# Kernel optimization log

Hardware: AMD Instinct MI355X
Metric: run time of the kernel (lower is better)

The kernel has to match this reference:

```python
import jax, jax.numpy as jnp
import numpy as np

K_SELECTED = 8  # config.num_selected_heads


def setup_inputs() -> dict:
    key = jax.random.key(0)
    k1, k2 = jax.random.split(key, 2)
    B, N, H, L = 4, 4096, 2048, 64
    x = jax.random.normal(k1, (B, N, H), dtype=jnp.float32)
    W_r = jax.random.normal(k2, (L, H), dtype=jnp.float32) * 0.02  # nn.Linear weight (L, H), no bias
    expert_bias = jnp.zeros((L,), dtype=jnp.float32)
    active_mask = jnp.ones((B, N), dtype=bool)
    return {"x": x, "W_r": W_r, "expert_bias": expert_bias, "active_mask": active_mask}


def reference(x, W_r, expert_bias, active_mask):
    L = expert_bias.shape[0]
    K = K_SELECTED
    # logits = x @ W_r.T  (bias-free routing projection)
    logits = jnp.einsum('bnh,lh->bnl', x, W_r)
    routing_scores = jax.nn.softmax(logits, axis=-1)            # unbiased probs
    biased_scores = jax.nn.softmax(logits + expert_bias, -1)    # biased probs for selection
    # top-K on biased scores -> selected head indices (B, N, K)
    _, selected_heads = jax.lax.top_k(biased_scores, K)
    # gather unbiased scores at selected indices and renormalize
    gathered = jnp.take_along_axis(routing_scores, selected_heads, axis=-1)
    routing_probs = gathered / gathered.sum(axis=-1, keepdims=True)
    # scatter into assignment mask: one-hot over L summed over K slots
    assignment_mask = jax.nn.one_hot(selected_heads, L, dtype=x.dtype).sum(axis=-2)  # (B, N, L)
    am = active_mask.astype(x.dtype)
    active_assignments = assignment_mask * am[..., None]
    num_active_assignments = am.sum() * K
    routing_freqs = active_assignments.sum(axis=(0, 1)) / num_active_assignments  # (L,)
    # LoadBalanceLoss.apply(expert_bias, routing_freqs): squared-imbalance value
    inv_L = 1.0 / L
    load_balance_loss = L * jnp.sum((routing_freqs - inv_L) ** 2)
    max_vio = jax.lax.stop_gradient(L * jnp.max(routing_freqs - inv_L))
    return selected_heads, routing_probs, load_balance_loss, max_vio
```

## Files before the change

kernel.cpp:

```cpp
#include <hip/hip_runtime.h>
#include <stdint.h>
#include <math.h>

constexpr int H     = 2048;
constexpr int L     = 64;
constexpr int K_SEL = 8;

constexpr int TMR   = 256;
constexpr int KS    = 8;
constexpr int KSLAB = H / KS;
constexpr int BK    = 32;
constexpr int SXR   = 260;
constexpr int SWR   = 68;

constexpr float EPS_GAP = 1e-4f;

constexpr int WS_COUNTS = 0;
constexpr int WS_NFIX   = 128;
constexpr int WS_LIST   = 256;
constexpr int WS_WT     = 16640;
constexpr int WS_LOGITS = 147712;

__global__ __launch_bounds__(256)
void prep(const float* __restrict__ Wr, float* __restrict__ Wt,
          unsigned int* __restrict__ wsu, float* __restrict__ logits)
{
    const int t = threadIdx.x, b = blockIdx.x;
    if (b == 32) {
        if (t < L + 1) wsu[WS_COUNTS + t] = 0u;
        if (t == 0)    wsu[WS_NFIX] = 0u;
        return;
    }
    if (b >= 33) {
        float4* p = (float4*)logits;
        const int zb = b - 33;
        #pragma unroll
        for (int q = 0; q < 16; ++q)
            p[(size_t)zb * 4096 + q * 256 + t] = make_float4(0.f, 0.f, 0.f, 0.f);
        return;
    }
    __shared__ float tile[64 * 65];
    const int k0 = b * 64;
    {
        const int l = t >> 2, kq = (t & 3) * 16;
        #pragma unroll
        for (int j = 0; j < 4; ++j) {
            float4 v = *(const float4*)(Wr + (size_t)l * H + k0 + kq + 4 * j);
            int k = kq + 4 * j;
            tile[(k + 0) * 65 + l] = v.x;
            tile[(k + 1) * 65 + l] = v.y;
            tile[(k + 2) * 65 + l] = v.z;
            tile[(k + 3) * 65 + l] = v.w;
        }
    }
    __syncthreads();
    {
        const int k = t >> 2, lq = (t & 3) * 16;
        #pragma unroll
        for (int j = 0; j < 4; ++j) {
            int l2 = lq + 4 * j;
            float4 o = make_float4(tile[k * 65 + l2], tile[k * 65 + l2 + 1],
                                   tile[k * 65 + l2 + 2], tile[k * 65 + l2 + 3]);
            *(float4*)(Wt + (size_t)(k0 + k) * L + l2) = o;
        }
    }
}

__global__ __launch_bounds__(256, 2)
void router_gemm(const float* __restrict__ x, const float* __restrict__ Wr,
                 float* __restrict__ logits)
{
    __shared__ __align__(16) float xs[BK * SXR];
    __shared__ __align__(16) float ws[BK * SWR];
    __shared__ __align__(16) float lg[64 * 65];

    const int t   = threadIdx.x;
    const int rb  = blockIdx.x & 63;
    const int ks  = blockIdx.x >> 6;
    const int R0  = rb * TMR;
    const int k0  = ks * KSLAB;
    const int g   = t >> 3;
    const int j   = t & 7;
    const int r0  = 8 * g, c0 = 8 * j;
    const int wid = t >> 6;
    const int lane = t & 63;

    float acc[8][8] = {};
    float4 xg[8], wg[2];

    const float* xp = x  + (size_t)(R0 + t) * H + k0;
    const float* wp = Wr + (size_t)lane * H     + k0 + 8 * wid;

    #pragma unroll
    for (int q = 0; q < 8; ++q) xg[q] = *(const float4*)(xp + 4 * q);
    wg[0] = *(const float4*)(wp);
    wg[1] = *(const float4*)(wp + 4);

    for (int s = 0; s < KSLAB / BK; ++s) {
        #pragma unroll
        for (int q = 0; q < 8; ++q) {
            const float4 v = xg[q];
            xs[(4 * q + 0) * SXR + t] = v.x;
            xs[(4 * q + 1) * SXR + t] = v.y;
            xs[(4 * q + 2) * SXR + t] = v.z;
            xs[(4 * q + 3) * SXR + t] = v.w;
        }
        #pragma unroll
        for (int e = 0; e < 2; ++e) {
            const float4 v = wg[e];
            const int kw = 8 * wid + 4 * e;
            ws[(kw + 0) * SWR + lane] = v.x;
            ws[(kw + 1) * SWR + lane] = v.y;
            ws[(kw + 2) * SWR + lane] = v.z;
            ws[(kw + 3) * SWR + lane] = v.w;
        }
        __syncthreads();

        if (s + 1 < KSLAB / BK) {
            const int kb = BK * (s + 1);
            #pragma unroll
            for (int q = 0; q < 8; ++q) xg[q] = *(const float4*)(xp + kb + 4 * q);
            wg[0] = *(const float4*)(wp + kb);
            wg[1] = *(const float4*)(wp + kb + 4);
        }

        #pragma unroll 8
        for (int kk = 0; kk < BK; ++kk) {
            const float4 xv0 = *(const float4*)(xs + kk * SXR + r0);
            const float4 xv1 = *(const float4*)(xs + kk * SXR + r0 + 4);
            const float4 wv0 = *(const float4*)(ws + kk * SWR + c0);
            const float4 wv1 = *(const float4*)(ws + kk * SWR + c0 + 4);
            const float xr[8] = {xv0.x, xv0.y, xv0.z, xv0.w, xv1.x, xv1.y, xv1.z, xv1.w};
            const float wc[8] = {wv0.x, wv0.y, wv0.z, wv0.w, wv1.x, wv1.y, wv1.z, wv1.w};
            #pragma unroll
            for (int i = 0; i < 8; ++i)
                #pragma unroll
                for (int jj = 0; jj < 8; ++jj)
                    acc[i][jj] = fmaf(xr[i], wc[jj], acc[i][jj]);
        }
        __syncthreads();
    }

    for (int c = 0; c < 4; ++c) {
        if (wid == c) {
            const int lr = 8 * (g & 7);
            #pragma unroll
            for (int i = 0; i < 8; ++i)
                #pragma unroll
                for (int jj = 0; jj < 8; ++jj)
                    lg[(lr + i) * 65 + c0 + jj] = acc[i][jj];
        }
        __syncthreads();
        float* dst = logits + (size_t)(R0 + 64 * c) * L;
        #pragma unroll
        for (int p = 0; p < 16; ++p) {
            const int idx = t + 256 * p;
            const int row = idx >> 6, col = idx & 63;
            atomicAdd(dst + (size_t)row * L + col, lg[row * 65 + col]);
        }
        __syncthreads();
    }
}

constexpr int TKR = 32;
__global__ __launch_bounds__(256)
void router_topk(const float* __restrict__ logits, const float* __restrict__ bias,
                 const unsigned char* __restrict__ am,
                 float* __restrict__ out_sel, float* __restrict__ out_probs,
                 unsigned int* __restrict__ g_counts, unsigned int* __restrict__ nfix,
                 unsigned int* __restrict__ list)
{
    __shared__ float bs[L];
    __shared__ unsigned int cnt[L + 1];

    const int t   = threadIdx.x;
    const int j   = t & 7;
    const int row = blockIdx.x * TKR + (t >> 3);

    if (t < L)     bs[t]  = bias[t];
    if (t < L + 1) cnt[t] = 0;
    __syncthreads();

    float rv[8], lv[8];
    {
        const float* lp = logits + (size_t)row * L + 8 * j;
        const float4 v0 = *(const float4*)(lp);
        const float4 v1 = *(const float4*)(lp + 4);
        rv[0] = v0.x; rv[1] = v0.y; rv[2] = v0.z; rv[3] = v0.w;
        rv[4] = v1.x; rv[5] = v1.y; rv[6] = v1.z; rv[7] = v1.w;
        #pragma unroll
        for (int i = 0; i < 8; ++i) lv[i] = rv[i] + bs[8 * j + i];
    }

    unsigned msk = 0;
    int   selidx[K_SEL];
    float selraw[K_SEL];
    float prev = 0.f, gmin = INFINITY;

    #pragma unroll
    for (int kk = 0; kk < K_SEL + 1; ++kk) {
        float best = -INFINITY; int bi = 1 << 30; float braw = 0.f;
        #pragma unroll
        for (int i = 0; i < 8; ++i) {
            const bool free_ = !((msk >> i) & 1u);
            if (free_ && lv[i] > best) { best = lv[i]; bi = 8 * j + i; braw = rv[i]; }
        }
        #pragma unroll
        for (int off = 1; off <= 4; off <<= 1) {
            const float ov  = __shfl_xor(best, off);
            const int   oi  = __shfl_xor(bi,   off);
            const float orw = __shfl_xor(braw, off);
            if (ov > best || (ov == best && oi < bi)) { best = ov; bi = oi; braw = orw; }
        }
        if (kk > 0) gmin = fminf(gmin, prev - best);
        prev = best;
        if (kk < K_SEL) {
            if ((bi >> 3) == j) msk |= 1u << (bi & 7);
            selidx[kk] = bi;
            selraw[kk] = braw;
        }
    }

    if (gmin < EPS_GAP) {
        if (j == 0) {
            unsigned int p = atomicAdd(nfix, 1u);
            list[p] = (unsigned int)row;
        }
    } else {
        float mx = -INFINITY;
        #pragma unroll
        for (int kk = 0; kk < K_SEL; ++kk) mx = fmaxf(mx, selraw[kk]);
        float e[K_SEL], ssum = 0.f;
        #pragma unroll
        for (int kk = 0; kk < K_SEL; ++kk) { e[kk] = expf(selraw[kk] - mx); ssum += e[kk]; }
        float myp = 0.f; int myi = 0;
        #pragma unroll
        for (int kk = 0; kk < K_SEL; ++kk)
            if (kk == j) { myp = e[kk] / ssum; myi = selidx[kk]; }
        out_sel  [(size_t)row * K_SEL + j] = (float)myi;
        out_probs[(size_t)row * K_SEL + j] = myp;
        if (am[row]) {
            atomicAdd(&cnt[myi], 1u);
            if (j == 0) atomicAdd(&cnt[L], 1u);
        }
    }
    __syncthreads();
    if (t < L + 1 && cnt[t]) atomicAdd(&g_counts[t], cnt[t]);
}

__global__ __launch_bounds__(256)
void fixup(const float* __restrict__ x, const float* __restrict__ Wt,
           const float* __restrict__ bias, const unsigned char* __restrict__ am,
           const unsigned int* __restrict__ nfix, const unsigned int* __restrict__ list,
           float* __restrict__ out_sel, float* __restrict__ out_probs,
           unsigned int* __restrict__ g_counts)
{
    const int lane = threadIdx.x & 63;
    const int wid  = (blockIdx.x << 2) | (threadIdx.x >> 6);
    const int nw   = gridDim.x << 2;
    const int n    = (int)*nfix;
    const double bl = (double)bias[lane];

    for (int i = wid; i < n; i += nw) {
        const int row = (int)list[i];
        const float* xr = x + (size_t)row * H;
        double a0 = 0.0, a1 = 0.0, a2 = 0.0, a3 = 0.0;
        #pragma unroll 2
        for (int k = 0; k < H; k += 16) {
            float4 x0 = *(const float4*)(xr + k);
            float4 x1 = *(const float4*)(xr + k + 4);
            float4 x2 = *(const float4*)(xr + k + 8);
            float4 x3 = *(const float4*)(xr + k + 12);
            a0 = fma((double)x0.x, (double)Wt[(k +  0) * L + lane], a0);
            a1 = fma((double)x0.y, (double)Wt[(k +  1) * L + lane], a1);
            a2 = fma((double)x0.z, (double)Wt[(k +  2) * L + lane], a2);
            a3 = fma((double)x0.w, (double)Wt[(k +  3) * L + lane], a3);
            a0 = fma((double)x1.x, (double)Wt[(k +  4) * L + lane], a0);
            a1 = fma((double)x1.y, (double)Wt[(k +  5) * L + lane], a1);
            a2 = fma((double)x1.z, (double)Wt[(k +  6) * L + lane], a2);
            a3 = fma((double)x1.w, (double)Wt[(k +  7) * L + lane], a3);
            a0 = fma((double)x2.x, (double)Wt[(k +  8) * L + lane], a0);
            a1 = fma((double)x2.y, (double)Wt[(k +  9) * L + lane], a1);
            a2 = fma((double)x2.z, (double)Wt[(k + 10) * L + lane], a2);
            a3 = fma((double)x2.w, (double)Wt[(k + 11) * L + lane], a3);
            a0 = fma((double)x3.x, (double)Wt[(k + 12) * L + lane], a0);
            a1 = fma((double)x3.y, (double)Wt[(k + 13) * L + lane], a1);
            a2 = fma((double)x3.z, (double)Wt[(k + 14) * L + lane], a2);
            a3 = fma((double)x3.w, (double)Wt[(k + 15) * L + lane], a3);
        }
        double acc = (a0 + a1) + (a2 + a3);

        double v = acc + bl;
        int    widx[K_SEL];
        double wlog[K_SEL];
        #pragma unroll
        for (int kk = 0; kk < K_SEL; ++kk) {
            double mv = v; int mi = lane;
            #pragma unroll
            for (int off = 32; off; off >>= 1) {
                double ov = __shfl_xor(mv, off);
                int    oi = __shfl_xor(mi, off);
                if (ov > mv || (ov == mv && oi < mi)) { mv = ov; mi = oi; }
            }
            widx[kk] = mi;
            wlog[kk] = __shfl(acc, mi);
            if (lane == mi) v = -INFINITY;
        }

        double mx = -INFINITY;
        #pragma unroll
        for (int kk = 0; kk < K_SEL; ++kk) mx = fmax(mx, wlog[kk]);
        float e[K_SEL], ssum = 0.f;
        #pragma unroll
        for (int kk = 0; kk < K_SEL; ++kk) { e[kk] = expf((float)(wlog[kk] - mx)); ssum += e[kk]; }

        if (lane < K_SEL) {
            out_sel[(size_t)row * K_SEL + lane]   = (float)widx[lane];
            out_probs[(size_t)row * K_SEL + lane] = e[lane] / ssum;
        }
        if (am[row]) {
            if (lane < K_SEL)  atomicAdd(&g_counts[widx[lane]], 1u);
            if (lane == K_SEL) atomicAdd(&g_counts[L], 1u);
        }
    }
}

__global__ void router_finalize(const unsigned int* __restrict__ g_counts,
                                float* __restrict__ out_scalars)
{
    const int l = threadIdx.x;
    const float denom = (float)g_counts[L] * (float)K_SEL;
    const float f = (float)g_counts[l] / denom;
    float d  = f - 1.0f / (float)L;
    float sq = d * d;
    #pragma unroll
    for (int o = 32; o > 0; o >>= 1) {
        sq += __shfl_down(sq, o);
        d = fmaxf(d, __shfl_down(d, o));
    }
    if (l == 0) {
        out_scalars[0] = (float)L * sq;
        out_scalars[1] = (float)L * d;
    }
}

extern "C" void kernel_launch(void* const* d_in, const int* in_sizes, int n_in,
                              void* d_out, int out_size, void* d_ws, size_t ws_size,
                              hipStream_t stream)
{
    const float* x          = (const float*)d_in[0];
    const float* Wr         = (const float*)d_in[1];
    const float* bias       = (const float*)d_in[2];
    const unsigned char* am = (const unsigned char*)d_in[3];
    float* out = (float*)d_out;
    float* wsf = (float*)d_ws;
    unsigned int* wsu = (unsigned int*)d_ws;

    const int rows = in_sizes[3];

    float* out_sel   = out;
    float* out_probs = out + (size_t)rows * K_SEL;
    float* out_scal  = out + (size_t)rows * K_SEL * 2;

    hipLaunchKernelGGL(prep,            dim3(97),                dim3(256), 0, stream,
                       Wr, wsf + WS_WT, wsu, wsf + WS_LOGITS);
    hipLaunchKernelGGL(router_gemm,     dim3((rows / TMR) * KS), dim3(256), 0, stream,
                       x, Wr, wsf + WS_LOGITS);
    hipLaunchKernelGGL(router_topk,     dim3(rows / TKR),        dim3(256), 0, stream,
                       wsf + WS_LOGITS, bias, am, out_sel, out_probs,
                       wsu + WS_COUNTS, wsu + WS_NFIX, wsu + WS_LIST);
    hipLaunchKernelGGL(fixup,           dim3(256),               dim3(256), 0, stream,
                       x, wsf + WS_WT, bias, am, wsu + WS_NFIX, wsu + WS_LIST,
                       out_sel, out_probs, wsu + WS_COUNTS);
    hipLaunchKernelGGL(router_finalize, dim3(1),                 dim3(64),  0, stream,
                       wsu + WS_COUNTS, out_scal);
}
```

Baseline: 296.9 us.

## Replace FP32 split-K GEMM with split-bf16 MFMA GEMM fused with top-k

Replaces the FP32 FMA router GEMM with a bf16 MFMA GEMM that emulates FP32 precision through a hi/lo split (three MFMAs per tile: hi*hi, hi*lo, lo*hi). W_r is pre-split into hi/lo bf16 in the prep kernel, and x is split on the fly while being staged into double-buffered shared memory. The top-k selection is fused into the same kernel, so logits stay in shared memory. This drops the split-K atomics, the zeroing of the logits buffer and the separate top-k launch. The trade-offs are a slightly reduced-precision product that may send more rows to the fixup path, and a small 32-row tile with one K-stage sync per iteration that may limit MFMA utilisation.

```diff
diff --git a/kernel.cpp b/kernel.cpp
--- a/kernel.cpp
+++ b/kernel.cpp
@@ -6,12 +6,10 @@
 constexpr int L     = 64;
 constexpr int K_SEL = 8;
 
-constexpr int TMR   = 256;
-constexpr int KS    = 8;
-constexpr int KSLAB = H / KS;
+constexpr int RPB   = 32;
 constexpr int BK    = 32;
-constexpr int SXR   = 260;
-constexpr int SWR   = 68;
+constexpr int NSTG  = H / BK;
+constexpr int SP    = 40;
 
 constexpr float EPS_GAP = 1e-4f;
 
@@ -19,11 +17,26 @@
 constexpr int WS_NFIX   = 128;
 constexpr int WS_LIST   = 256;
 constexpr int WS_WT     = 16640;
-constexpr int WS_LOGITS = 147712;
+constexpr int WS_WHC    = 147712;
+constexpr int WS_WLC    = 213248;
+
+typedef __attribute__((ext_vector_type(8))) short bf16x8;
+typedef __attribute__((ext_vector_type(4))) float f32x4;
+
+__device__ __forceinline__ void cvt_hi_lo(float c, short& h, short& l)
+{
+    unsigned u  = __float_as_uint(c);
+    unsigned hb = (u + 0x7fffu + ((u >> 16) & 1u)) >> 16;
+    float hf    = __uint_as_float(hb << 16);
+    float lof   = c - hf;
+    h = (short)hb;
+    l = (short)(__float_as_uint(lof) >> 16);
+}
 
 __global__ __launch_bounds__(256)
 void prep(const float* __restrict__ Wr, float* __restrict__ Wt,
-          unsigned int* __restrict__ wsu, float* __restrict__ logits)
+          unsigned int* __restrict__ wsu, short* __restrict__ whc,
+          short* __restrict__ wlc)
 {
     const int t = threadIdx.x, b = blockIdx.x;
     if (b == 32) {
@@ -32,11 +45,24 @@
         return;
     }
     if (b >= 33) {
-        float4* p = (float4*)logits;
-        const int zb = b - 33;
-        #pragma unroll
-        for (int q = 0; q < 16; ++q)
-            p[(size_t)zb * 4096 + q * 256 + t] = make_float4(0.f, 0.f, 0.f, 0.f);
+        const int z = b - 33;
+        const int e = 2 * z + (t >> 7);
+        const int idx = t & 127;
+        #pragma unroll
+        for (int u = 0; u < 4; ++u) {
+            const int f4i = idx + 128 * u;
+            const int k   = 4 * f4i;
+            const float4 v = ((const float4*)(Wr + (size_t)e * H))[f4i];
+            short4 hh, ll;
+            cvt_hi_lo(v.x, hh.x, ll.x);
+            cvt_hi_lo(v.y, hh.y, ll.y);
+            cvt_hi_lo(v.z, hh.z, ll.z);
+            cvt_hi_lo(v.w, hh.w, ll.w);
+            const int c  = k >> 5, kk = k & 31;
+            const int di = (c * 64 + e) * 32 + kk;
+            *(short4*)(whc + di) = hh;
+            *(short4*)(wlc + di) = ll;
+        }
         return;
     }
     __shared__ float tile[64 * 65];
@@ -67,181 +93,172 @@
 }
 
 __global__ __launch_bounds__(256, 2)
-void router_gemm(const float* __restrict__ x, const float* __restrict__ Wr,
-                 float* __restrict__ logits)
-{
-    __shared__ __align__(16) float xs[BK * SXR];
-    __shared__ __align__(16) float ws[BK * SWR];
-    __shared__ __align__(16) float lg[64 * 65];
-
-    const int t   = threadIdx.x;
-    const int rb  = blockIdx.x & 63;
-    const int ks  = blockIdx.x >> 6;
-    const int R0  = rb * TMR;
-    const int k0  = ks * KSLAB;
-    const int g   = t >> 3;
-    const int j   = t & 7;
-    const int r0  = 8 * g, c0 = 8 * j;
-    const int wid = t >> 6;
-    const int lane = t & 63;
-
-    float acc[8][8] = {};
-    float4 xg[8], wg[2];
-
-    const float* xp = x  + (size_t)(R0 + t) * H + k0;
-    const float* wp = Wr + (size_t)lane * H     + k0 + 8 * wid;
-
-    #pragma unroll
-    for (int q = 0; q < 8; ++q) xg[q] = *(const float4*)(xp + 4 * q);
-    wg[0] = *(const float4*)(wp);
-    wg[1] = *(const float4*)(wp + 4);
-
-    for (int s = 0; s < KSLAB / BK; ++s) {
-        #pragma unroll
-        for (int q = 0; q < 8; ++q) {
-            const float4 v = xg[q];
-            xs[(4 * q + 0) * SXR + t] = v.x;
-            xs[(4 * q + 1) * SXR + t] = v.y;
-            xs[(4 * q + 2) * SXR + t] = v.z;
-            xs[(4 * q + 3) * SXR + t] = v.w;
-        }
-        #pragma unroll
-        for (int e = 0; e < 2; ++e) {
-            const float4 v = wg[e];
-            const int kw = 8 * wid + 4 * e;
-            ws[(kw + 0) * SWR + lane] = v.x;
-            ws[(kw + 1) * SWR + lane] = v.y;
-            ws[(kw + 2) * SWR + lane] = v.z;
-            ws[(kw + 3) * SWR + lane] = v.w;
-        }
-        __syncthreads();
-
-        if (s + 1 < KSLAB / BK) {
-            const int kb = BK * (s + 1);
-            #pragma unroll
-            for (int q = 0; q < 8; ++q) xg[q] = *(const float4*)(xp + kb + 4 * q);
-            wg[0] = *(const float4*)(wp + kb);
-            wg[1] = *(const float4*)(wp + kb + 4);
-        }
-
-        #pragma unroll 8
-        for (int kk = 0; kk < BK; ++kk) {
-            const float4 xv0 = *(const float4*)(xs + kk * SXR + r0);
-            const float4 xv1 = *(const float4*)(xs + kk * SXR + r0 + 4);
-            const float4 wv0 = *(const float4*)(ws + kk * SWR + c0);
-            const float4 wv1 = *(const float4*)(ws + kk * SWR + c0 + 4);
-            const float xr[8] = {xv0.x, xv0.y, xv0.z, xv0.w, xv1.x, xv1.y, xv1.z, xv1.w};
-            const float wc[8] = {wv0.x, wv0.y, wv0.z, wv0.w, wv1.x, wv1.y, wv1.z, wv1.w};
-            #pragma unroll
-            for (int i = 0; i < 8; ++i)
-                #pragma unroll
-                for (int jj = 0; jj < 8; ++jj)
-                    acc[i][jj] = fmaf(xr[i], wc[jj], acc[i][jj]);
-        }
-        __syncthreads();
-    }
-
-    for (int c = 0; c < 4; ++c) {
-        if (wid == c) {
-            const int lr = 8 * (g & 7);
-            #pragma unroll
-            for (int i = 0; i < 8; ++i)
-                #pragma unroll
-                for (int jj = 0; jj < 8; ++jj)
-                    lg[(lr + i) * 65 + c0 + jj] = acc[i][jj];
-        }
-        __syncthreads();
-        float* dst = logits + (size_t)(R0 + 64 * c) * L;
-        #pragma unroll
-        for (int p = 0; p < 16; ++p) {
-            const int idx = t + 256 * p;
-            const int row = idx >> 6, col = idx & 63;
-            atomicAdd(dst + (size_t)row * L + col, lg[row * 65 + col]);
-        }
-        __syncthreads();
-    }
-}
-
-constexpr int TKR = 32;
-__global__ __launch_bounds__(256)
-void router_topk(const float* __restrict__ logits, const float* __restrict__ bias,
+void router_mfma(const float* __restrict__ x, const short* __restrict__ whc,
+                 const short* __restrict__ wlc, const float* __restrict__ bias,
                  const unsigned char* __restrict__ am,
                  float* __restrict__ out_sel, float* __restrict__ out_probs,
                  unsigned int* __restrict__ g_counts, unsigned int* __restrict__ nfix,
                  unsigned int* __restrict__ list)
 {
+    __shared__ __align__(16) short sxh[2][RPB * SP];
+    __shared__ __align__(16) short sxl[2][RPB * SP];
+    __shared__ __align__(16) short swh[2][L * SP];
+    __shared__ __align__(16) short swl[2][L * SP];
+    __shared__ __align__(16) float lg[RPB * 68];
     __shared__ float bs[L];
     __shared__ unsigned int cnt[L + 1];
 
-    const int t   = threadIdx.x;
-    const int j   = t & 7;
-    const int row = blockIdx.x * TKR + (t >> 3);
+    const int t  = threadIdx.x;
+    const int R0 = blockIdx.x * RPB;
 
     if (t < L)     bs[t]  = bias[t];
     if (t < L + 1) cnt[t] = 0;
+
+    const int lw  = t & 63, w = t >> 6;
+    const int r0l = 16 * (w & 1);
+    const int n0  = 32 * (w >> 1);
+    const int fr  = lw & 15;
+    const int kg  = lw >> 4;
+    const int kb  = 8 * kg;
+
+    const float*  xp  = x + (size_t)(R0 + (t >> 3)) * H + 4 * (t & 7);
+    const float4* whp = (const float4*)whc + t;
+    const float4* wlp = (const float4*)wlc + t;
+
+    f32x4 acc[2] = {};
+    float4 xg, wh_r, wl_r;
+
+    xg   = *(const float4*)(xp);
+    wh_r = whp[0];
+    wl_r = wlp[0];
+    {
+        short4 h4, l4;
+        cvt_hi_lo(xg.x, h4.x, l4.x);
+        cvt_hi_lo(xg.y, h4.y, l4.y);
+        cvt_hi_lo(xg.z, h4.z, l4.z);
+        cvt_hi_lo(xg.w, h4.w, l4.w);
+        const int xi = (t >> 3) * SP + 4 * (t & 7);
+        *(short4*)&sxh[0][xi] = h4;
+        *(short4*)&sxl[0][xi] = l4;
+        const int wi = (t >> 2) * SP + 8 * (t & 3);
+        *(float4*)&swh[0][wi] = wh_r;
+        *(float4*)&swl[0][wi] = wl_r;
+    }
     __syncthreads();
-
-    float rv[8], lv[8];
+    xg   = *(const float4*)(xp + BK);
+    wh_r = whp[256];
+    wl_r = wlp[256];
+
+    for (int s = 0; s < NSTG; ++s) {
+        const int p = s & 1;
+        if (s + 1 < NSTG) {
+            short4 h4, l4;
+            cvt_hi_lo(xg.x, h4.x, l4.x);
+            cvt_hi_lo(xg.y, h4.y, l4.y);
+            cvt_hi_lo(xg.z, h4.z, l4.z);
+            cvt_hi_lo(xg.w, h4.w, l4.w);
+            const int xi = (t >> 3) * SP + 4 * (t & 7);
+            *(short4*)&sxh[p ^ 1][xi] = h4;
+            *(short4*)&sxl[p ^ 1][xi] = l4;
+            const int wi = (t >> 2) * SP + 8 * (t & 3);
+            *(float4*)&swh[p ^ 1][wi] = wh_r;
+            *(float4*)&swl[p ^ 1][wi] = wl_r;
+        }
+        if (s + 2 < NSTG) {
+            xg   = *(const float4*)(xp + BK * (s + 2));
+            wh_r = whp[256 * (s + 2)];
+            wl_r = wlp[256 * (s + 2)];
+        }
+        {
+            const bf16x8 ah = *(const bf16x8*)&sxh[p][(r0l + fr) * SP + kb];
+            const bf16x8 al = *(const bf16x8*)&sxl[p][(r0l + fr) * SP + kb];
+            #pragma unroll
+            for (int tt = 0; tt < 2; ++tt) {
+                const int nc = (n0 + 16 * tt + fr) * SP + kb;
+                const bf16x8 bh = *(const bf16x8*)&swh[p][nc];
+                const bf16x8 bl = *(const bf16x8*)&swl[p][nc];
+                acc[tt] = __builtin_amdgcn_mfma_f32_16x16x32_bf16(ah, bh, acc[tt], 0, 0, 0);
+                acc[tt] = __builtin_amdgcn_mfma_f32_16x16x32_bf16(ah, bl, acc[tt], 0, 0, 0);
+                acc[tt] = __builtin_amdgcn_mfma_f32_16x16x32_bf16(al, bh, acc[tt], 0, 0, 0);
+            }
+        }
+        __syncthreads();
+    }
+
+    #pragma unroll
+    for (int tt = 0; tt < 2; ++tt)
+        #pragma unroll
+        for (int r = 0; r < 4; ++r)
+            lg[(r0l + 4 * kg + r) * 68 + n0 + 16 * tt + fr] = acc[tt][r];
+    __syncthreads();
+
     {
-        const float* lp = logits + (size_t)row * L + 8 * j;
-        const float4 v0 = *(const float4*)(lp);
-        const float4 v1 = *(const float4*)(lp + 4);
-        rv[0] = v0.x; rv[1] = v0.y; rv[2] = v0.z; rv[3] = v0.w;
-        rv[4] = v1.x; rv[5] = v1.y; rv[6] = v1.z; rv[7] = v1.w;
-        #pragma unroll
-        for (int i = 0; i < 8; ++i) lv[i] = rv[i] + bs[8 * j + i];
-    }
-
-    unsigned msk = 0;
-    int   selidx[K_SEL];
-    float selraw[K_SEL];
-    float prev = 0.f, gmin = INFINITY;
-
-    #pragma unroll
-    for (int kk = 0; kk < K_SEL + 1; ++kk) {
-        float best = -INFINITY; int bi = 1 << 30; float braw = 0.f;
-        #pragma unroll
-        for (int i = 0; i < 8; ++i) {
-            const bool free_ = !((msk >> i) & 1u);
-            if (free_ && lv[i] > best) { best = lv[i]; bi = 8 * j + i; braw = rv[i]; }
-        }
-        #pragma unroll
-        for (int off = 1; off <= 4; off <<= 1) {
-            const float ov  = __shfl_xor(best, off);
-            const int   oi  = __shfl_xor(bi,   off);
-            const float orw = __shfl_xor(braw, off);
-            if (ov > best || (ov == best && oi < bi)) { best = ov; bi = oi; braw = orw; }
-        }
-        if (kk > 0) gmin = fminf(gmin, prev - best);
-        prev = best;
-        if (kk < K_SEL) {
-            if ((bi >> 3) == j) msk |= 1u << (bi & 7);
-            selidx[kk] = bi;
-            selraw[kk] = braw;
-        }
-    }
-
-    if (gmin < EPS_GAP) {
-        if (j == 0) {
-            unsigned int p = atomicAdd(nfix, 1u);
-            list[p] = (unsigned int)row;
-        }
-    } else {
-        float mx = -INFINITY;
-        #pragma unroll
-        for (int kk = 0; kk < K_SEL; ++kk) mx = fmaxf(mx, selraw[kk]);
-        float e[K_SEL], ssum = 0.f;
-        #pragma unroll
-        for (int kk = 0; kk < K_SEL; ++kk) { e[kk] = expf(selraw[kk] - mx); ssum += e[kk]; }
-        float myp = 0.f; int myi = 0;
-        #pragma unroll
-        for (int kk = 0; kk < K_SEL; ++kk)
-            if (kk == j) { myp = e[kk] / ssum; myi = selidx[kk]; }
-        out_sel  [(size_t)row * K_SEL + j] = (float)myi;
-        out_probs[(size_t)row * K_SEL + j] = myp;
-        if (am[row]) {
-            atomicAdd(&cnt[myi], 1u);
-            if (j == 0) atomicAdd(&cnt[L], 1u);
+        const int tj   = t & 7;
+        const int lrow = t >> 3;
+        const int grow = R0 + lrow;
+
+        float rv[8], lv[8];
+        {
+            const float* lp = &lg[lrow * 68 + 8 * tj];
+            const float4 v0 = *(const float4*)(lp);
+            const float4 v1 = *(const float4*)(lp + 4);
+            rv[0] = v0.x; rv[1] = v0.y; rv[2] = v0.z; rv[3] = v0.w;
+            rv[4] = v1.x; rv[5] = v1.y; rv[6] = v1.z; rv[7] = v1.w;
+            #pragma unroll
+            for (int i = 0; i < 8; ++i) lv[i] = rv[i] + bs[8 * tj + i];
+        }
+
+        unsigned msk = 0;
+        int   selidx[K_SEL];
+        float selraw[K_SEL];
+        float prev = 0.f, gmin = INFINITY;
+
+        #pragma unroll
+        for (int kk = 0; kk < K_SEL + 1; ++kk) {
+            float best = -INFINITY; int bi = 1 << 30; float braw = 0.f;
+            #pragma unroll
+            for (int i = 0; i < 8; ++i) {
+                const bool free_ = !((msk >> i) & 1u);
+                if (free_ && lv[i] > best) { best = lv[i]; bi = 8 * tj + i; braw = rv[i]; }
+            }
+            #pragma unroll
+            for (int off = 1; off <= 4; off <<= 1) {
+                const float ov  = __shfl_xor(best, off);
+                const int   oi  = __shfl_xor(bi,   off);
+                const float orw = __shfl_xor(braw, off);
+                if (ov > best || (ov == best && oi < bi)) { best = ov; bi = oi; braw = orw; }
+            }
+            if (kk > 0) gmin = fminf(gmin, prev - best);
+            prev = best;
+            if (kk < K_SEL) {
+                if ((bi >> 3) == tj) msk |= 1u << (bi & 7);
+                selidx[kk] = bi;
+                selraw[kk] = braw;
+            }
+        }
+
+        if (gmin < EPS_GAP) {
+            if (tj == 0) {
+                unsigned int pp = atomicAdd(nfix, 1u);
+                list[pp] = (unsigned int)grow;
+            }
+        } else {
+            float mx = -INFINITY;
+            #pragma unroll
+            for (int kk = 0; kk < K_SEL; ++kk) mx = fmaxf(mx, selraw[kk]);
+            float e[K_SEL], ssum = 0.f;
+            #pragma unroll
+            for (int kk = 0; kk < K_SEL; ++kk) { e[kk] = expf(selraw[kk] - mx); ssum += e[kk]; }
+            float myp = 0.f; int myi = 0;
+            #pragma unroll
+            for (int kk = 0; kk < K_SEL; ++kk)
+                if (kk == tj) { myp = e[kk] / ssum; myi = selidx[kk]; }
+            out_sel  [(size_t)grow * K_SEL + tj] = (float)myi;
+            out_probs[(size_t)grow * K_SEL + tj] = myp;
+            if (am[grow]) {
+                atomicAdd(&cnt[myi], 1u);
+                if (tj == 0) atomicAdd(&cnt[L], 1u);
+            }
         }
     }
     __syncthreads();
@@ -362,16 +379,17 @@
     float* out_probs = out + (size_t)rows * K_SEL;
     float* out_scal  = out + (size_t)rows * K_SEL * 2;
 
-    hipLaunchKernelGGL(prep,            dim3(97),                dim3(256), 0, stream,
-                       Wr, wsf + WS_WT, wsu, wsf + WS_LOGITS);
-    hipLaunchKernelGGL(router_gemm,     dim3((rows / TMR) * KS), dim3(256), 0, stream,
-                       x, Wr, wsf + WS_LOGITS);
-    hipLaunchKernelGGL(router_topk,     dim3(rows / TKR),        dim3(256), 0, stream,
-                       wsf + WS_LOGITS, bias, am, out_sel, out_probs,
+    short* whc = (short*)(wsu + WS_WHC);
+    short* wlc = (short*)(wsu + WS_WLC);
+
+    hipLaunchKernelGGL(prep,            dim3(65),         dim3(256), 0, stream,
+                       Wr, wsf + WS_WT, wsu, whc, wlc);
+    hipLaunchKernelGGL(router_mfma,     dim3(rows / RPB), dim3(256), 0, stream,
+                       x, whc, wlc, bias, am, out_sel, out_probs,
                        wsu + WS_COUNTS, wsu + WS_NFIX, wsu + WS_LIST);
-    hipLaunchKernelGGL(fixup,           dim3(256),               dim3(256), 0, stream,
+    hipLaunchKernelGGL(fixup,           dim3(256),        dim3(256), 0, stream,
                        x, wsf + WS_WT, bias, am, wsu + WS_NFIX, wsu + WS_LIST,
                        out_sel, out_probs, wsu + WS_COUNTS);
-    hipLaunchKernelGGL(router_finalize, dim3(1),                 dim3(64),  0, stream,
+    hipLaunchKernelGGL(router_finalize, dim3(1),          dim3(64),  0, stream,
                        wsu + WS_COUNTS, out_scal);
 }
```

Result: faster. 281.2 us (-5.3%).
